# Performance work log

Hardware: AMD Instinct MI355X
Metric: run time of the kernel (lower is better)

The kernel has to match this reference:

```python
import jax, jax.numpy as jnp
import numpy as np
import math

B, N, NX, NY, HID = 131072, 6, 8, 8, 32
NB = NX * NY
NOCC = 3

_MATCHINGS_6 = [((0,1),(2,3),(4,5)), ((0,1),(2,4),(3,5)), ((0,1),(2,5),(3,4)),
                ((0,2),(1,3),(4,5)), ((0,2),(1,4),(3,5)), ((0,2),(1,5),(3,4)),
                ((0,3),(1,2),(4,5)), ((0,3),(1,4),(2,5)), ((0,3),(1,5),(2,4)),
                ((0,4),(1,2),(3,5)), ((0,4),(1,3),(2,5)), ((0,4),(1,5),(2,3)),
                ((0,5),(1,2),(3,4)), ((0,5),(1,3),(2,4)), ((0,5),(1,4),(2,3))]

def _matching_signs():
    out = []
    for m in _MATCHINGS_6:
        perm = [k for pair in m for k in pair]
        inv = sum(1 for a in range(6) for b in range(a + 1, 6) if perm[a] > perm[b])
        out.append((-1.0) ** inv)
    return np.array(out, np.float32)

_I = np.array([[p[0] for p in m] for m in _MATCHINGS_6])  # (15, 3)
_J = np.array([[p[1] for p in m] for m in _MATCHINGS_6])  # (15, 3)
_S = _matching_signs()                                     # (15,)

def _pfaffian6(A):
    # A: (B, 6, 6) antisymmetric -> (B,). 15-term combinatorial Pfaffian sum.
    terms = jnp.prod(A[:, _I, _J], axis=-1)               # (B, 15)
    return terms @ jnp.asarray(_S, A.dtype)

# 2D harmonic-oscillator (Hermite-Gaussian) basis, nx*ny functions.
_NORM = np.array([1.0 / math.sqrt(2.0 ** m * math.factorial(m) * math.sqrt(math.pi))
                  for m in range(max(NX, NY))], np.float32)

def _hermite(t, n):
    # physicists' Hermite polynomials H_0..H_{n-1}, stacked on last axis
    H = [jnp.ones_like(t)]
    if n > 1:
        H.append(2.0 * t)
    for k in range(2, n):
        H.append(2.0 * t * H[-1] - 2.0 * (k - 1) * H[-2])
    return jnp.stack(H[:n], axis=-1)

def _basis(x):
    # x: (B, N, 2) -> Phi: (B, N, NX*NY)
    u, v = x[..., 0], x[..., 1]
    Hx = _hermite(u, NX) * _NORM[:NX]
    Hy = _hermite(v, NY) * _NORM[:NY]
    g = jnp.exp(-0.5 * (u * u + v * v))
    Phi = Hx[..., :, None] * Hy[..., None, :] * g[..., None, None]
    return Phi.reshape(x.shape[0], x.shape[1], NX * NY)

def _forward(x, spin, F_ud, F_uu_raw, F_dd_raw, W1, b1, W2, b2, W3, b3, scale):
    dt = x.dtype
    Phi = _basis(x)                                        # (B, 6, NB)
    F_uu = F_uu_raw - F_uu_raw.T
    F_dd = F_dd_raw - F_dd_raw.T
    def pair(F):
        return jnp.einsum('bik,bjk->bij', Phi @ F, Phi)    # (B, 6, 6)
    A_uu, A_dd, A_ud = pair(F_uu), pair(F_dd), pair(F_ud)
    up = spin == 0
    dn = spin == 1
    uu = (up[:, :, None] & up[:, None, :]).astype(dt)
    dd = (dn[:, :, None] & dn[:, None, :]).astype(dt)
    ud = (up[:, :, None] & dn[:, None, :]).astype(dt)
    du = (dn[:, :, None] & up[:, None, :]).astype(dt)
    A = A_uu * uu + A_dd * dd + A_ud * ud - jnp.swapaxes(A_ud, 1, 2) * du
    # PairCorrectionMLP: features (dx, dy, r2, same_spin)
    dx = x[:, :, None, :] - x[:, None, :, :]               # (B, 6, 6, 2)
    r2 = jnp.sum(dx * dx, axis=-1, keepdims=True)
    same = (spin[:, :, None] == spin[:, None, :]).astype(dt)[..., None]
    feat = jnp.concatenate([dx, r2, same], axis=-1)        # (B, 6, 6, 4)
    h = jax.nn.silu(feat @ W1 + b1)
    h = jax.nn.silu(h @ W2 + b2)
    out = (h @ W3 + b3)[..., 0]                            # (B, 6, 6)
    A = A + scale * (out - jnp.swapaxes(out, 1, 2))
    pf = _pfaffian6(A)                                     # (B,)
    sign = jnp.where(pf == 0, jnp.ones_like(pf), jnp.sign(pf))
    logabs = 0.5 * jnp.log(pf * pf + 1e-60)
    return sign, logabs

def setup_inputs() -> dict:
    key = jax.random.key(0)
    ks = jax.random.split(key, 8)
    x = jax.random.normal(ks[0], (B, N, 2), jnp.float32)
    spin = jax.random.randint(ks[1], (B, N), 0, 2)
    C = 0.3 * jax.random.normal(ks[2], (NB, NOCC), jnp.float32)
    F_ud = C @ C.T                                         # occupied-space projector init
    F_uu_raw = 0.01 * jax.random.normal(ks[3], (NB, NB), jnp.float32)
    F_dd_raw = 0.01 * jax.random.normal(ks[4], (NB, NB), jnp.float32)
    W1 = 0.5 * jax.random.normal(ks[5], (4, HID), jnp.float32)
    b1 = jnp.zeros((HID,), jnp.float32)
    W2 = jax.random.normal(ks[6], (HID, HID), jnp.float32) / math.sqrt(HID)
    b2 = jnp.zeros((HID,), jnp.float32)
    W3 = 0.1 * jax.random.normal(ks[7], (HID, 1), jnp.float32)
    b3 = jnp.zeros((1,), jnp.float32)
    scale = jnp.float32(0.01)
    return {"x": x, "spin": spin, "F_ud": F_ud, "F_uu_raw": F_uu_raw,
            "F_dd_raw": F_dd_raw, "W1": W1, "b1": b1, "W2": W2, "b2": b2,
            "W3": W3, "b3": b3, "scale": scale}

def reference(x, spin, F_ud, F_uu_raw, F_dd_raw, W1, b1, W2, b2, W3, b3, scale):
    return _forward(x, spin, F_ud, F_uu_raw, F_dd_raw, W1, b1, W2, b2, W3, b3, scale)
```

## Files before the change

### kernel.cpp

```cpp
#include <hip/hip_runtime.h>
#include <math.h>

typedef float vf4 __attribute__((ext_vector_type(4)));
typedef float vf2 __attribute__((ext_vector_type(2)));

#define B_TOTAL 131072
#define WPB 8
#define BLOCK_T (WPB * 64)

__device__ __forceinline__ float rfl_f(float v) {
    return __int_as_float(__builtin_amdgcn_readfirstlane(__float_as_int(v)));
}

__device__ __forceinline__ float herm_sel(float t, int m) {
    float h0 = 1.0f;
    float h1 = 2.0f * t;
    float r = (m == 0) ? h0 : h1;
#pragma unroll
    for (int d = 2; d < 8; ++d) {
        float hk = 2.0f * t * h1 - (2.0f * (float)(d - 1)) * h0;
        r = (m == d) ? hk : r;
        h0 = h1;
        h1 = hk;
    }
    return r;
}

__device__ __forceinline__ float norm_of(int m) {
    double f = 1.0;
#pragma unroll
    for (int d = 2; d < 8; ++d) f = (d <= m) ? f * (double)d : f;
    double p2 = (double)(1 << m);
    double sp = sqrt(3.14159265358979323846);
    return (float)(1.0 / sqrt((p2 * f) * sp));
}

__device__ __forceinline__ float sel6f(const float* a, int m) {
    float r = a[0];
    r = (m == 1) ? a[1] : r;
    r = (m == 2) ? a[2] : r;
    r = (m == 3) ? a[3] : r;
    r = (m == 4) ? a[4] : r;
    r = (m == 5) ? a[5] : r;
    return r;
}

__device__ __forceinline__ int sel6i(const int* a, int m) {
    int r = a[0];
    r = (m == 1) ? a[1] : r;
    r = (m == 2) ? a[2] : r;
    r = (m == 3) ? a[3] : r;
    r = (m == 4) ? a[4] : r;
    r = (m == 5) ? a[5] : r;
    return r;
}

extern "C" __global__ void __launch_bounds__(BLOCK_T, 4)
pfaffA(const float* __restrict__ x, const int* __restrict__ spin,
       const float* __restrict__ Fud, const float* __restrict__ Fuu,
       const float* __restrict__ Fdd, float* __restrict__ wsAp)
{
    __shared__ alignas(16) float sFuu[4096];
    __shared__ alignas(16) float sFdd[4096];
    __shared__ alignas(16) float sPhiC[WPB][3][32];

    const int tid = threadIdx.x;

    for (int idx = tid; idx < 4096; idx += BLOCK_T) {
        int l = idx >> 6, k = idx & 63;
        int tr = k * 64 + l;
        sFuu[idx] = Fuu[idx] - Fuu[tr];
        sFdd[idx] = Fdd[idx] - Fdd[tr];
    }
    __syncthreads();

    const int wid = tid >> 6;
    const int lane = tid & 63;
    const int b = blockIdx.x * WPB + wid;

    float u[6], v[6];
    int sp6[6];
#pragma unroll
    for (int i = 0; i < 6; ++i) {
        u[i] = rfl_f(x[b * 12 + 2 * i]);
        v[i] = rfl_f(x[b * 12 + 2 * i + 1]);
        sp6[i] = __builtin_amdgcn_readfirstlane(spin[b * 6 + i]);
    }

    const int mx = lane >> 3, my = lane & 7;
    const float nx = norm_of(mx), ny = norm_of(my);
    float Phi[6];
#pragma unroll
    for (int i = 0; i < 6; ++i) {
        float t = u[i] * u[i] + v[i] * v[i];
        float g = expf(-0.5f * t);
        float hxn = herm_sel(u[i], mx) * nx;
        float hyn = herm_sel(v[i], my) * ny;
        Phi[i] = (hxn * hyn) * g;
    }

    vf2 auu[3] = {{0.f,0.f},{0.f,0.f},{0.f,0.f}};
    vf2 add2[3] = {{0.f,0.f},{0.f,0.f},{0.f,0.f}};
    vf2 aud[3] = {{0.f,0.f},{0.f,0.f},{0.f,0.f}};
    const float* fxb = Fud + lane;
    const int cl = lane & 15;
#pragma unroll 1
    for (int c = 0; c < 4; ++c) {
        asm volatile("s_waitcnt lgkmcnt(0)" ::: "memory");
        __builtin_amdgcn_sched_barrier(0);
        if ((lane >> 4) == c) {
#pragma unroll
            for (int i = 0; i < 6; ++i)
                sPhiC[wid][i >> 1][cl * 2 + (i & 1)] = Phi[i];
        }
        asm volatile("s_waitcnt lgkmcnt(0)" ::: "memory");
        __builtin_amdgcn_sched_barrier(0);

#pragma unroll
        for (int l2 = 0; l2 < 16; l2 += 2) {
            const int l = c * 16 + l2;
            vf4 pq0 = *(const vf4*)&sPhiC[wid][0][l2 * 2];
            vf4 pq1 = *(const vf4*)&sPhiC[wid][1][l2 * 2];
            vf4 pq2 = *(const vf4*)&sPhiC[wid][2][l2 * 2];
#pragma unroll
            for (int d = 0; d < 2; ++d) {
                float fu = sFuu[(l + d) * 64 + lane];
                float fd = sFdd[(l + d) * 64 + lane];
                float fx = fxb[(l2 + d) * 64];
                vf2 fu2 = {fu, fu}, fd2 = {fd, fd}, fx2 = {fx, fx};
                vf2 p0 = {pq0[2 * d], pq0[2 * d + 1]};
                vf2 p1 = {pq1[2 * d], pq1[2 * d + 1]};
                vf2 p2 = {pq2[2 * d], pq2[2 * d + 1]};
                auu[0] = __builtin_elementwise_fma(p0, fu2, auu[0]);
                auu[1] = __builtin_elementwise_fma(p1, fu2, auu[1]);
                auu[2] = __builtin_elementwise_fma(p2, fu2, auu[2]);
                add2[0] = __builtin_elementwise_fma(p0, fd2, add2[0]);
                add2[1] = __builtin_elementwise_fma(p1, fd2, add2[1]);
                add2[2] = __builtin_elementwise_fma(p2, fd2, add2[2]);
                aud[0] = __builtin_elementwise_fma(p0, fx2, aud[0]);
                aud[1] = __builtin_elementwise_fma(p1, fx2, aud[1]);
                aud[2] = __builtin_elementwise_fma(p2, fx2, aud[2]);
            }
        }
        fxb += 1024;
    }
    float puu[6], pdd[6], pud[6];
#pragma unroll
    for (int c = 0; c < 3; ++c) {
        puu[2 * c] = auu[c][0];  puu[2 * c + 1] = auu[c][1];
        pdd[2 * c] = add2[c][0]; pdd[2 * c + 1] = add2[c][1];
        pud[2 * c] = aud[c][0];  pud[2 * c + 1] = aud[c][1];
    }

    float myAp = 0.0f;
    {
        int pidx = 0;
#pragma unroll
        for (int i = 0; i < 6; ++i) {
#pragma unroll
            for (int j = i + 1; j < 6; ++j) {
                int si = sp6[i], sj = sp6[j];
                bool du = (si == 1) && (sj == 0);
                float rowv = (si == 0) ? ((sj == 0) ? puu[i] : pud[i])
                                       : ((sj == 1) ? pdd[i] : pud[j]);
                float colv = du ? Phi[i] : Phi[j];
                float prod = rowv * colv;
                prod = du ? -prod : prod;
#pragma unroll
                for (int m = 32; m >= 1; m >>= 1)
                    prod += __shfl_xor(prod, m, 64);
                myAp = (lane == pidx) ? prod : myAp;
                ++pidx;
            }
        }
    }
    if (lane < 15) wsAp[b * 16 + lane] = myAp;
}

extern "C" __global__ void __launch_bounds__(512, 6)
pfaffB(const float* __restrict__ x, const int* __restrict__ spin,
       const float* __restrict__ W1, const float* __restrict__ b1,
       const float* __restrict__ W2, const float* __restrict__ b2,
       const float* __restrict__ W3, const float* __restrict__ b3,
       const float* __restrict__ scale_p, const float* __restrict__ wsAp,
       float* __restrict__ out)
{
    const int tid = threadIdx.x;
    const int half = tid >> 5;
    const int p = tid & 31;
    const int b = blockIdx.x * 16 + half;

    int i = p / 5;
    int r5 = p - i * 5;
    int j = r5 + ((r5 >= i) ? 1 : 0);
    i = min(i, 5);
    j = min(j, 5);

    float xi = x[b * 12 + 2 * i], yi = x[b * 12 + 2 * i + 1];
    float xj = x[b * 12 + 2 * j], yj = x[b * 12 + 2 * j + 1];
    int si = spin[b * 6 + i], sj = spin[b * 6 + j];

    float dx = xi - xj;
    float dy = yi - yj;
    float r2 = dx * dx + dy * dy;
    float same = (si == sj) ? 1.0f : 0.0f;
    vf2 dx2 = {dx, dx}, dy2 = {dy, dy}, r22 = {r2, r2}, sm2 = {same, same};

    float h1v[32];
#pragma unroll
    for (int h = 0; h < 32; h += 2) {
        vf2 a = *(const vf2*)&b1[h];
        a = __builtin_elementwise_fma(dx2, *(const vf2*)&W1[h], a);
        a = __builtin_elementwise_fma(dy2, *(const vf2*)&W1[32 + h], a);
        a = __builtin_elementwise_fma(r22, *(const vf2*)&W1[64 + h], a);
        a = __builtin_elementwise_fma(sm2, *(const vf2*)&W1[96 + h], a);
#pragma unroll
        for (int s = 0; s < 2; ++s) {
            float av = a[s];
            float e = __expf(-av);
            h1v[h + s] = __fdividef(av, 1.0f + e);
        }
    }
    float o = b3[0];
    for (int h2 = 0; h2 < 32; h2 += 2) {
        vf2 a0 = *(const vf2*)&b2[h2];
        vf2 a1 = {0.f, 0.f}, a2 = {0.f, 0.f}, a3 = {0.f, 0.f};
#pragma unroll
        for (int l = 0; l < 32; l += 4) {
            vf2 m0 = {h1v[l + 0], h1v[l + 0]};
            vf2 m1 = {h1v[l + 1], h1v[l + 1]};
            vf2 m2 = {h1v[l + 2], h1v[l + 2]};
            vf2 m3 = {h1v[l + 3], h1v[l + 3]};
            a0 = __builtin_elementwise_fma(m0, *(const vf2*)&W2[(l + 0) * 32 + h2], a0);
            a1 = __builtin_elementwise_fma(m1, *(const vf2*)&W2[(l + 1) * 32 + h2], a1);
            a2 = __builtin_elementwise_fma(m2, *(const vf2*)&W2[(l + 2) * 32 + h2], a2);
            a3 = __builtin_elementwise_fma(m3, *(const vf2*)&W2[(l + 3) * 32 + h2], a3);
        }
        vf2 a = (a0 + a1) + (a2 + a3);
#pragma unroll
        for (int s = 0; s < 2; ++s) {
            float av = a[s];
            float e = __expf(-av);
            float sil = __fdividef(av, 1.0f + e);
            o = fmaf(sil, W3[h2 + s], o);
        }
    }

    const int t = p & 15;
    const unsigned long long TI = 0x0433222111100000ull;
    const unsigned long long TJ = 0x0554543543254321ull;
    int i2 = (int)((TI >> (4 * t)) & 15);
    int j2 = (int)((TJ >> (4 * t)) & 15);
    float o_ij = __shfl(o, i2 * 5 + (j2 - 1), 32);
    float o_ji = __shfl(o, j2 * 5 + i2, 32);
    const float scl = scale_p[0];
    float ApV = wsAp[b * 16 + t];
    float Af = ApV + scl * (o_ij - o_ji);

    const unsigned long long TA = 0x0444333222111000ull;
    const unsigned long long TB = 0x0765865875876BA9ull;
    const unsigned long long TC = 0x09AC9BDABECDECDEull;
    int ia = (int)((TA >> (4 * t)) & 15);
    int ib = (int)((TB >> (4 * t)) & 15);
    int ic = (int)((TC >> (4 * t)) & 15);
    double Afa = (double)__shfl(Af, ia, 32);
    double Afb = (double)__shfl(Af, ib, 32);
    double Afc = (double)__shfl(Af, ic, 32);
    double pd = Afa * Afb * Afc;
    pd = (t & 1) ? -pd : pd;
    pd = (p < 15) ? pd : 0.0;
#pragma unroll
    for (int m = 16; m >= 1; m >>= 1)
        pd += __shfl_xor(pd, m, 32);

    if (p == 0) {
        float pf = (float)pd;
        float sg = (pf == 0.0f) ? 1.0f : ((pf > 0.0f) ? 1.0f : -1.0f);
        float tt = pf * pf;
        float la = 0.5f * logf(tt);
        out[b] = sg;
        out[B_TOTAL + b] = la;
    }
}

extern "C" __global__ void __launch_bounds__(BLOCK_T, 4)
pfaff6_full(const float* __restrict__ x, const int* __restrict__ spin,
            const float* __restrict__ Fud, const float* __restrict__ Fuu,
            const float* __restrict__ Fdd,
            const float* __restrict__ W1, const float* __restrict__ b1,
            const float* __restrict__ W2, const float* __restrict__ b2,
            const float* __restrict__ W3, const float* __restrict__ b3,
            const float* __restrict__ scale_p,
            float* __restrict__ out)
{
    __shared__ alignas(16) float sFuu[4096];
    __shared__ alignas(16) float sFdd[4096];
    __shared__ alignas(16) float sFud[4096];
    __shared__ alignas(16) float sPhi2[WPB][3][128];
    __shared__ float sOut[WPB][32];

    const int tid = threadIdx.x;
    for (int idx = tid; idx < 4096; idx += BLOCK_T) {
        int l = idx >> 6, k = idx & 63;
        int tr = k * 64 + l;
        sFuu[idx] = Fuu[idx] - Fuu[tr];
        sFdd[idx] = Fdd[idx] - Fdd[tr];
        sFud[idx] = Fud[idx];
    }
    __syncthreads();

    const int wid = tid >> 6;
    const int lane = tid & 63;
    const int b = blockIdx.x * WPB + wid;

    float u[6], v[6];
    int sp6[6];
#pragma unroll
    for (int i = 0; i < 6; ++i) {
        u[i] = rfl_f(x[b * 12 + 2 * i]);
        v[i] = rfl_f(x[b * 12 + 2 * i + 1]);
        sp6[i] = __builtin_amdgcn_readfirstlane(spin[b * 6 + i]);
    }

    const int mx = lane >> 3, my = lane & 7;
    const float nx = norm_of(mx), ny = norm_of(my);
    float Phi[6];
#pragma unroll
    for (int i = 0; i < 6; ++i) {
        float t = u[i] * u[i] + v[i] * v[i];
        float g = expf(-0.5f * t);
        float ph = ((herm_sel(u[i], mx) * nx) * (herm_sel(v[i], my) * ny)) * g;
        Phi[i] = ph;
        sPhi2[wid][i >> 1][lane * 2 + (i & 1)] = ph;
    }
    asm volatile("s_waitcnt lgkmcnt(0)" ::: "memory");
    __builtin_amdgcn_sched_barrier(0);

    vf2 auu[3] = {{0.f,0.f},{0.f,0.f},{0.f,0.f}};
    vf2 add2[3] = {{0.f,0.f},{0.f,0.f},{0.f,0.f}};
    vf2 aud[3] = {{0.f,0.f},{0.f,0.f},{0.f,0.f}};
    for (int l2 = 0; l2 < 64; l2 += 2) {
        vf4 pq0 = *(const vf4*)&sPhi2[wid][0][l2 * 2];
        vf4 pq1 = *(const vf4*)&sPhi2[wid][1][l2 * 2];
        vf4 pq2 = *(const vf4*)&sPhi2[wid][2][l2 * 2];
#pragma unroll
        for (int d = 0; d < 2; ++d) {
            int l = l2 + d;
            float fu = sFuu[l * 64 + lane];
            float fd = sFdd[l * 64 + lane];
            float fx = sFud[l * 64 + lane];
            vf2 fu2 = {fu, fu}, fd2 = {fd, fd}, fx2 = {fx, fx};
            vf2 p0 = {pq0[2 * d], pq0[2 * d + 1]};
            vf2 p1 = {pq1[2 * d], pq1[2 * d + 1]};
            vf2 p2 = {pq2[2 * d], pq2[2 * d + 1]};
            auu[0] = __builtin_elementwise_fma(p0, fu2, auu[0]);
            auu[1] = __builtin_elementwise_fma(p1, fu2, auu[1]);
            auu[2] = __builtin_elementwise_fma(p2, fu2, auu[2]);
            add2[0] = __builtin_elementwise_fma(p0, fd2, add2[0]);
            add2[1] = __builtin_elementwise_fma(p1, fd2, add2[1]);
            add2[2] = __builtin_elementwise_fma(p2, fd2, add2[2]);
            aud[0] = __builtin_elementwise_fma(p0, fx2, aud[0]);
            aud[1] = __builtin_elementwise_fma(p1, fx2, aud[1]);
            aud[2] = __builtin_elementwise_fma(p2, fx2, aud[2]);
        }
    }
    float puu[6], pdd[6], pud[6];
#pragma unroll
    for (int c = 0; c < 3; ++c) {
        puu[2 * c] = auu[c][0];  puu[2 * c + 1] = auu[c][1];
        pdd[2 * c] = add2[c][0]; pdd[2 * c + 1] = add2[c][1];
        pud[2 * c] = aud[c][0];  pud[2 * c + 1] = aud[c][1];
    }

    float Ap[15];
    {
        int pidx = 0;
#pragma unroll
        for (int i = 0; i < 6; ++i) {
#pragma unroll
            for (int j = i + 1; j < 6; ++j) {
                int si = sp6[i], sj = sp6[j];
                bool du = (si == 1) && (sj == 0);
                float rowv = (si == 0) ? ((sj == 0) ? puu[i] : pud[i])
                                       : ((sj == 1) ? pdd[i] : pud[j]);
                float colv = du ? Phi[i] : Phi[j];
                float prod = rowv * colv;
                prod = du ? -prod : prod;
#pragma unroll
                for (int m = 32; m >= 1; m >>= 1)
                    prod += __shfl_xor(prod, m, 64);
                Ap[pidx++] = rfl_f(prod);
            }
        }
    }

    {
        int p = lane;
        int i = p / 5;
        int r5 = p - i * 5;
        int j = r5 + ((r5 >= i) ? 1 : 0);
        i = min(i, 5);
        j = min(j, 5);
        float dx = sel6f(u, i) - sel6f(u, j);
        float dy = sel6f(v, i) - sel6f(v, j);
        float r2 = dx * dx + dy * dy;
        float same = (sel6i(sp6, i) == sel6i(sp6, j)) ? 1.0f : 0.0f;
        vf2 dx2 = {dx, dx}, dy2 = {dy, dy}, r22 = {r2, r2}, sm2 = {same, same};

        float h1v[32];
#pragma unroll
        for (int h = 0; h < 32; h += 2) {
            vf2 a = *(const vf2*)&b1[h];
            a = __builtin_elementwise_fma(dx2, *(const vf2*)&W1[h], a);
            a = __builtin_elementwise_fma(dy2, *(const vf2*)&W1[32 + h], a);
            a = __builtin_elementwise_fma(r22, *(const vf2*)&W1[64 + h], a);
            a = __builtin_elementwise_fma(sm2, *(const vf2*)&W1[96 + h], a);
#pragma unroll
            for (int s = 0; s < 2; ++s) {
                float av = a[s];
                float e = __expf(-av);
                h1v[h + s] = __fdividef(av, 1.0f + e);
            }
        }
        float o = b3[0];
        for (int h2 = 0; h2 < 32; h2 += 2) {
            vf2 a0 = *(const vf2*)&b2[h2];
            vf2 a1 = {0.f, 0.f}, a2 = {0.f, 0.f}, a3 = {0.f, 0.f};
#pragma unroll
            for (int l = 0; l < 32; l += 4) {
                vf2 m0 = {h1v[l + 0], h1v[l + 0]};
                vf2 m1 = {h1v[l + 1], h1v[l + 1]};
                vf2 m2 = {h1v[l + 2], h1v[l + 2]};
                vf2 m3 = {h1v[l + 3], h1v[l + 3]};
                a0 = __builtin_elementwise_fma(m0, *(const vf2*)&W2[(l + 0) * 32 + h2], a0);
                a1 = __builtin_elementwise_fma(m1, *(const vf2*)&W2[(l + 1) * 32 + h2], a1);
                a2 = __builtin_elementwise_fma(m2, *(const vf2*)&W2[(l + 2) * 32 + h2], a2);
                a3 = __builtin_elementwise_fma(m3, *(const vf2*)&W2[(l + 3) * 32 + h2], a3);
            }
            vf2 a = (a0 + a1) + (a2 + a3);
#pragma unroll
            for (int s = 0; s < 2; ++s) {
                float av = a[s];
                float e = __expf(-av);
                float sil = __fdividef(av, 1.0f + e);
                o = fmaf(sil, W3[h2 + s], o);
            }
        }
        if (p < 30) sOut[wid][p] = o;
    }
    asm volatile("s_waitcnt lgkmcnt(0)" ::: "memory");
    __builtin_amdgcn_sched_barrier(0);

    const float scl = rfl_f(scale_p[0]);
    float Af[15];
    {
        int pidx = 0;
#pragma unroll
        for (int i = 0; i < 6; ++i) {
#pragma unroll
            for (int j = i + 1; j < 6; ++j) {
                float o_ij = sOut[wid][i * 5 + (j - 1)];
                float o_ji = sOut[wid][j * 5 + i];
                Af[pidx] = Ap[pidx] + scl * (o_ij - o_ji);
                ++pidx;
            }
        }
    }
    {
        double pfd = 0.0;
#define PFT(sgn, a, bb, c) pfd += (sgn) * ((double)Af[a] * (double)Af[bb] * (double)Af[c]);
        PFT( 1.0, 0, 9, 14) PFT(-1.0, 0, 10, 13) PFT( 1.0, 0, 11, 12)
        PFT(-1.0, 1, 6, 14) PFT( 1.0, 1, 7, 13)  PFT(-1.0, 1, 8, 12)
        PFT( 1.0, 2, 5, 14) PFT(-1.0, 2, 7, 11)  PFT( 1.0, 2, 8, 10)
        PFT(-1.0, 3, 5, 13) PFT( 1.0, 3, 6, 11)  PFT(-1.0, 3, 8, 9)
        PFT( 1.0, 4, 5, 12) PFT(-1.0, 4, 6, 10)  PFT( 1.0, 4, 7, 9)
#undef PFT
        if (lane == 0) {
            float pf = (float)pfd;
            float sg = (pf == 0.0f) ? 1.0f : ((pf > 0.0f) ? 1.0f : -1.0f);
            float t = pf * pf;
            float la = 0.5f * logf(t);
            out[b] = sg;
            out[B_TOTAL + b] = la;
        }
    }
}

extern "C" void kernel_launch(void* const* d_in, const int* in_sizes, int n_in,
                              void* d_out, int out_size, void* d_ws, size_t ws_size,
                              hipStream_t stream) {
    const float* x     = (const float*)d_in[0];
    const int*   spin  = (const int*)d_in[1];
    const float* Fud   = (const float*)d_in[2];
    const float* Fuu   = (const float*)d_in[3];
    const float* Fdd   = (const float*)d_in[4];
    const float* W1    = (const float*)d_in[5];
    const float* b1    = (const float*)d_in[6];
    const float* W2    = (const float*)d_in[7];
    const float* b2    = (const float*)d_in[8];
    const float* W3    = (const float*)d_in[9];
    const float* b3    = (const float*)d_in[10];
    const float* scale = (const float*)d_in[11];
    float* out = (float*)d_out;

    const size_t wsNeed = (size_t)B_TOTAL * 16 * sizeof(float);
    if (ws_size >= wsNeed) {
        float* wsAp = (float*)d_ws;
        hipLaunchKernelGGL(pfaffA, dim3(B_TOTAL / WPB), dim3(BLOCK_T), 0, stream,
                           x, spin, Fud, Fuu, Fdd, wsAp);
        hipLaunchKernelGGL(pfaffB, dim3(B_TOTAL / 16), dim3(512), 0, stream,
                           x, spin, W1, b1, W2, b2, W3, b3, scale, wsAp, out);
    } else {
        hipLaunchKernelGGL(pfaff6_full, dim3(B_TOTAL / WPB), dim3(BLOCK_T), 0, stream,
                           x, spin, Fud, Fuu, Fdd, W1, b1, W2, b2, W3, b3, scale, out);
    }
}
```

Before: 643.9 us.

## Precompute transposed antisymmetric F matrices in a prep kernel, drop LDS staging

Adds a small prep kernel that builds the antisymmetrized Fuu and Fdd and copies Fud into a transposed, lane-contiguous layout in workspace. The main kernel then skips the per-block 32KB LDS fill and the syncthreads, and reads F columns directly from global/L2 as 16-byte vector loads per lane. The aim is to remove redundant per-block antisymmetrization and LDS traffic and to raise occupancy by freeing LDS. The cost is an extra kernel launch, plus strided per-lane global loads that depend on cache hits instead of LDS.

```diff
diff --git a/kernel.cpp b/kernel.cpp
--- a/kernel.cpp
+++ b/kernel.cpp
@@ -55,25 +55,29 @@
     return r;
 }
 
+extern "C" __global__ void __launch_bounds__(256)
+pfaffPrep(const float* __restrict__ Fud, const float* __restrict__ Fuu,
+          const float* __restrict__ Fdd, float* __restrict__ ws)
+{
+    int idx = blockIdx.x * 256 + threadIdx.x;
+    int m = idx >> 12;
+    int e = idx & 4095;
+    int k = e >> 6, l = e & 63;
+    float vv;
+    if (m == 0)      vv = Fuu[l * 64 + k] - Fuu[k * 64 + l];
+    else if (m == 1) vv = Fdd[l * 64 + k] - Fdd[k * 64 + l];
+    else             vv = Fud[l * 64 + k];
+    ws[idx] = vv;
+}
+
 extern "C" __global__ void __launch_bounds__(BLOCK_T, 4)
 pfaffA(const float* __restrict__ x, const int* __restrict__ spin,
-       const float* __restrict__ Fud, const float* __restrict__ Fuu,
-       const float* __restrict__ Fdd, float* __restrict__ wsAp)
+       const float* __restrict__ Tuu, const float* __restrict__ Tdd,
+       const float* __restrict__ Tud, float* __restrict__ wsAp)
 {
-    __shared__ alignas(16) float sFuu[4096];
-    __shared__ alignas(16) float sFdd[4096];
     __shared__ alignas(16) float sPhiC[WPB][3][32];
 
     const int tid = threadIdx.x;
-
-    for (int idx = tid; idx < 4096; idx += BLOCK_T) {
-        int l = idx >> 6, k = idx & 63;
-        int tr = k * 64 + l;
-        sFuu[idx] = Fuu[idx] - Fuu[tr];
-        sFdd[idx] = Fdd[idx] - Fdd[tr];
-    }
-    __syncthreads();
-
     const int wid = tid >> 6;
     const int lane = tid & 63;
     const int b = blockIdx.x * WPB + wid;
@@ -102,7 +106,9 @@
     vf2 auu[3] = {{0.f,0.f},{0.f,0.f},{0.f,0.f}};
     vf2 add2[3] = {{0.f,0.f},{0.f,0.f},{0.f,0.f}};
     vf2 aud[3] = {{0.f,0.f},{0.f,0.f},{0.f,0.f}};
-    const float* fxb = Fud + lane;
+    const float* fub = Tuu + lane * 64;
+    const float* fdb = Tdd + lane * 64;
+    const float* fxb = Tud + lane * 64;
     const int cl = lane & 15;
 #pragma unroll 1
     for (int c = 0; c < 4; ++c) {
@@ -117,32 +123,39 @@
         __builtin_amdgcn_sched_barrier(0);
 
 #pragma unroll
-        for (int l2 = 0; l2 < 16; l2 += 2) {
-            const int l = c * 16 + l2;
-            vf4 pq0 = *(const vf4*)&sPhiC[wid][0][l2 * 2];
-            vf4 pq1 = *(const vf4*)&sPhiC[wid][1][l2 * 2];
-            vf4 pq2 = *(const vf4*)&sPhiC[wid][2][l2 * 2];
-#pragma unroll
-            for (int d = 0; d < 2; ++d) {
-                float fu = sFuu[(l + d) * 64 + lane];
-                float fd = sFdd[(l + d) * 64 + lane];
-                float fx = fxb[(l2 + d) * 64];
-                vf2 fu2 = {fu, fu}, fd2 = {fd, fd}, fx2 = {fx, fx};
-                vf2 p0 = {pq0[2 * d], pq0[2 * d + 1]};
-                vf2 p1 = {pq1[2 * d], pq1[2 * d + 1]};
-                vf2 p2 = {pq2[2 * d], pq2[2 * d + 1]};
-                auu[0] = __builtin_elementwise_fma(p0, fu2, auu[0]);
-                auu[1] = __builtin_elementwise_fma(p1, fu2, auu[1]);
-                auu[2] = __builtin_elementwise_fma(p2, fu2, auu[2]);
-                add2[0] = __builtin_elementwise_fma(p0, fd2, add2[0]);
-                add2[1] = __builtin_elementwise_fma(p1, fd2, add2[1]);
-                add2[2] = __builtin_elementwise_fma(p2, fd2, add2[2]);
-                aud[0] = __builtin_elementwise_fma(p0, fx2, aud[0]);
-                aud[1] = __builtin_elementwise_fma(p1, fx2, aud[1]);
-                aud[2] = __builtin_elementwise_fma(p2, fx2, aud[2]);
-            }
-        }
-        fxb += 1024;
+        for (int l4 = 0; l4 < 16; l4 += 4) {
+            vf4 fuq = *(const vf4*)&fub[l4];
+            vf4 fdq = *(const vf4*)&fdb[l4];
+            vf4 fxq = *(const vf4*)&fxb[l4];
+#pragma unroll
+            for (int e = 0; e < 2; ++e) {
+                const int lp = l4 + 2 * e;
+                vf4 pq0 = *(const vf4*)&sPhiC[wid][0][lp * 2];
+                vf4 pq1 = *(const vf4*)&sPhiC[wid][1][lp * 2];
+                vf4 pq2 = *(const vf4*)&sPhiC[wid][2][lp * 2];
+#pragma unroll
+                for (int d = 0; d < 2; ++d) {
+                    const int dd = 2 * e + d;
+                    float fu = fuq[dd];
+                    float fd = fdq[dd];
+                    float fx = fxq[dd];
+                    vf2 fu2 = {fu, fu}, fd2 = {fd, fd}, fx2 = {fx, fx};
+                    vf2 p0 = {pq0[2 * d], pq0[2 * d + 1]};
+                    vf2 p1 = {pq1[2 * d], pq1[2 * d + 1]};
+                    vf2 p2 = {pq2[2 * d], pq2[2 * d + 1]};
+                    auu[0] = __builtin_elementwise_fma(p0, fu2, auu[0]);
+                    auu[1] = __builtin_elementwise_fma(p1, fu2, auu[1]);
+                    auu[2] = __builtin_elementwise_fma(p2, fu2, auu[2]);
+                    add2[0] = __builtin_elementwise_fma(p0, fd2, add2[0]);
+                    add2[1] = __builtin_elementwise_fma(p1, fd2, add2[1]);
+                    add2[2] = __builtin_elementwise_fma(p2, fd2, add2[2]);
+                    aud[0] = __builtin_elementwise_fma(p0, fx2, aud[0]);
+                    aud[1] = __builtin_elementwise_fma(p1, fx2, aud[1]);
+                    aud[2] = __builtin_elementwise_fma(p2, fx2, aud[2]);
+                }
+            }
+        }
+        fub += 16; fdb += 16; fxb += 16;
     }
     float puu[6], pdd[6], pud[6];
 #pragma unroll
@@ -503,11 +516,14 @@
     const float* scale = (const float*)d_in[11];
     float* out = (float*)d_out;
 
-    const size_t wsNeed = (size_t)B_TOTAL * 16 * sizeof(float);
+    const size_t wsNeed = (size_t)(12288 + B_TOTAL * 16) * sizeof(float);
     if (ws_size >= wsNeed) {
-        float* wsAp = (float*)d_ws;
+        float* T     = (float*)d_ws;
+        float* wsAp  = T + 12288;
+        hipLaunchKernelGGL(pfaffPrep, dim3(48), dim3(256), 0, stream,
+                           Fud, Fuu, Fdd, T);
         hipLaunchKernelGGL(pfaffA, dim3(B_TOTAL / WPB), dim3(BLOCK_T), 0, stream,
-                           x, spin, Fud, Fuu, Fdd, wsAp);
+                           x, spin, T, T + 4096, T + 8192, wsAp);
         hipLaunchKernelGGL(pfaffB, dim3(B_TOTAL / 16), dim3(512), 0, stream,
                            x, spin, W1, b1, W2, b2, W3, b3, scale, wsAp, out);
     } else {
```

New measurement: 1.021 ms. 1.59x slower.
